# Performance work log

Measured on AMD Instinct MI355X. Metric: run time of the kernel, lower is better.

Reference implementation:

```python
import jax, jax.numpy as jnp
import numpy as np
from jax.scipy.linalg import solve_triangular

X_DIM, N_INEQ, N_EQ = 64, 32, 16
N = X_DIM + N_INEQ      # primal+slack dim = 96
M = N_EQ + N_INEQ       # combined constraint count = 48
GAMMA = 2.0
NUM_STEPS = 10
BOUND = 1000.0          # state_slack_bound
BATCH = 4096


def setup_inputs() -> dict:
    key = jax.random.key(0)
    k1, k2, k3, k4, k5 = jax.random.split(key, 5)
    x = jax.random.normal(k1, (BATCH, N), dtype=jnp.float32)
    parms = jax.random.normal(k2, (BATCH, X_DIM + N_EQ + N_INEQ), dtype=jnp.float32)
    # PSD quadratic objective matrix so Md = gamma/2*I + Hf is PD for Cholesky
    Qh = jax.random.normal(k3, (X_DIM, X_DIM), dtype=jnp.float32) * 0.1
    Q = Qh @ Qh.T + jnp.eye(X_DIM, dtype=jnp.float32)
    A = jax.random.normal(k4, (N_EQ, X_DIM), dtype=jnp.float32) * 0.1
    G = jax.random.normal(k5, (N_INEQ, X_DIM), dtype=jnp.float32) * 0.1
    return {"x": x, "parms": parms, "Q": Q, "A": A, "G": G}


def _prox_g1(xs, parms, Q, A, G):
    # prox of g1(x,s) = f(x) + i_{F(x,s)=0} via 2nd-order obj / 1st-order constraint approx
    def f_single(z, p):
        xv = z[:X_DIM]
        return 0.5 * xv @ Q @ xv + p[:X_DIM] @ xv

    def F_single(z, p):
        xv, s = z[:X_DIM], z[X_DIM:]
        return jnp.concatenate([A @ xv - p[X_DIM:X_DIM + N_EQ],
                                G @ xv + s - p[X_DIM + N_EQ:]])

    # torch version computes JF/QR under no_grad -> stop_gradient here
    JFx = jax.lax.stop_gradient(jax.vmap(jax.jacrev(F_single, argnums=0))(xs, parms))  # [B,M,N]
    Qc, Rc = jnp.linalg.qr(jnp.swapaxes(JFx, 1, 2), mode='complete')  # Qc [B,N,N], Rc [B,N,M]
    Rr = Rc[:, :M, :]       # [B,M,M]
    Qr = Qc[:, :, :M]       # range space  [B,N,M]
    Qn = Qc[:, :, M:]       # null space   [B,N,N-M]

    Hf = jax.vmap(jax.hessian(f_single, argnums=0))(xs, parms)  # [B,N,N]
    Md = (GAMMA / 2) * jnp.eye(N, dtype=xs.dtype) + Hf          # metric defaults to identity
    QTMdQ = jnp.einsum('bni,bnm,bmj->bij', Qn, Md, Qn)          # [B,N-M,N-M]
    Lcho = jnp.linalg.cholesky(QTMdQ)

    Fx = jax.vmap(F_single)(xs, parms)                 # [B,M]
    b = -Fx[..., None] + JFx @ xs[..., None]           # [B,M,1]
    zeta_r = solve_triangular(jnp.swapaxes(Rr, 1, 2), b, lower=True)
    zeta = Qr @ zeta_r                                 # particular solution [B,N,1]

    fg = jax.vmap(jax.grad(f_single, argnums=0))(xs, parms)[..., None]
    zq = Md @ (xs[..., None] - zeta) - (GAMMA / 2) * fg
    zq = jnp.swapaxes(Qn, 1, 2) @ zq
    zq = solve_triangular(Lcho, zq, lower=True)
    zq = solve_triangular(jnp.swapaxes(Lcho, 1, 2), zq, lower=False)
    zq = Qn @ zq
    return (zq + zeta)[..., 0]


def _prox_g2(v):
    # box projection: x in [-BOUND, BOUND], slacks in [0, BOUND]
    l = jnp.concatenate([-BOUND * jnp.ones(X_DIM, dtype=v.dtype),
                         jnp.zeros(N_INEQ, dtype=v.dtype)])
    u = BOUND * jnp.ones(N, dtype=v.dtype)
    return l + jax.nn.relu(u - l - jax.nn.relu(u - v))


def reference(x, parms, Q, A, G):
    y = x
    for _ in range(NUM_STEPS):  # Douglas-Rachford fixed-point iteration
        y = _prox_g1(x, parms, Q, A, G)
        z = _prox_g2(2.0 * y - x)
        x = x + z - y
    return y[:, :X_DIM]  # primal solution estimate
```

## Files before the change

### kernel.cpp

```cpp
#include <hip/hip_runtime.h>


typedef __attribute__((ext_vector_type(8))) short short8v;
typedef __attribute__((ext_vector_type(4))) short short4v;
typedef __attribute__((ext_vector_type(4))) float float4v;

#define MFMA_BF16 __builtin_amdgcn_mfma_f32_16x16x32_bf16

__device__ __forceinline__ void ld4(const float* p, float* d) {
  float4 v = *(const float4*)p;
  d[0] = v.x; d[1] = v.y; d[2] = v.z; d[3] = v.w;
}
__device__ __forceinline__ void st4(float* p, const float* s) {
  *(float4*)p = make_float4(s[0], s[1], s[2], s[3]);
}
__device__ __forceinline__ float fastrcp(float x) {
  float r = __builtin_amdgcn_rcpf(x);
  return r * (2.0f - x * r);
}
__device__ __forceinline__ void mm4(float W[4][4], const float A[4][4], const float B[4][4]) {
  #pragma unroll
  for (int r = 0; r < 4; ++r)
    #pragma unroll
    for (int q = 0; q < 4; ++q) {
      float s = A[r][0]*B[0][q];
      #pragma unroll
      for (int k = 1; k < 4; ++k) s += A[r][k]*B[k][q];
      W[r][q] = s;
    }
}
__device__ __forceinline__ void inv4(float D[4][4]) {
  #pragma unroll
  for (int p = 0; p < 4; ++p) {
    float pi = fastrcp(D[p][p]);
    D[p][p] = pi;
    #pragma unroll
    for (int q = 0; q < 4; ++q) if (q != p) D[p][q] *= pi;
    #pragma unroll
    for (int i = 0; i < 4; ++i) if (i != p) {
      float f = D[i][p];
      #pragma unroll
      for (int q = 0; q < 4; ++q) if (q != p) D[i][q] -= f * D[p][q];
      D[i][p] = -f * pi;
    }
  }
}
__device__ __forceinline__ unsigned short bf16h_rne(float v) {
  unsigned u = __float_as_uint(v);
  unsigned r = u + 0x7FFFu + ((u >> 16) & 1u);
  return (unsigned short)(r >> 16);
}
__device__ __forceinline__ float bf16_back(unsigned short h) {
  return __uint_as_float(((unsigned)h) << 16);
}
__device__ __forceinline__ void split8(const float v[8], short8v &hi, short8v &lo) {
  #pragma unroll
  for (int j = 0; j < 8; ++j) {
    unsigned short h = bf16h_rne(v[j]);
    hi[j] = (short)h;
    lo[j] = (short)bf16h_rne(v[j] - bf16_back(h));
  }
}

__device__ __forceinline__ void gj_step64(const float* __restrict__ src,
                                          float* __restrict__ dst,
                                          int b, int ig, int jg) {
  float D[4][4], C[4][4], R[4][4], T4[4][4], W[4][4];
  #pragma unroll
  for (int r = 0; r < 4; ++r) {
    ld4(&src[(4*b + r)*68 + 4*b],  D[r]);
    ld4(&src[(4*ig + r)*68 + 4*b], C[r]);
    ld4(&src[(4*b + r)*68 + 4*jg], R[r]);
    ld4(&src[(4*ig + r)*68 + 4*jg], T4[r]);
  }
  inv4(D);
  if (ig == b) {
    if (jg == b) {
      #pragma unroll
      for (int r = 0; r < 4; ++r)
        #pragma unroll
        for (int q = 0; q < 4; ++q) W[r][q] = D[r][q];
    } else {
      mm4(W, D, R);
    }
  } else {
    float E[4][4];
    mm4(E, C, D);
    if (jg == b) {
      #pragma unroll
      for (int r = 0; r < 4; ++r)
        #pragma unroll
        for (int q = 0; q < 4; ++q) W[r][q] = -E[r][q];
    } else {
      #pragma unroll
      for (int r = 0; r < 4; ++r)
        #pragma unroll
        for (int q = 0; q < 4; ++q) {
          float s = T4[r][q];
          #pragma unroll
          for (int k = 0; k < 4; ++k) s -= E[r][k] * R[k][q];
          W[r][q] = s;
        }
    }
  }
  #pragma unroll
  for (int r = 0; r < 4; ++r) st4(&dst[(4*ig + r)*68 + 4*jg], W[r]);
  __syncthreads();
}

__device__ __forceinline__ void gj_step48(const float* __restrict__ src,
                                          float* __restrict__ dst,
                                          int b, int tid) {
  const bool act = tid < 144;
  const int ig = tid / 12, jg = tid - (tid / 12) * 12;
  float D[4][4], C[4][4], R[4][4], T4[4][4], W[4][4];
  if (act) {
    #pragma unroll
    for (int r = 0; r < 4; ++r) {
      ld4(&src[(4*b + r)*52 + 4*b],  D[r]);
      ld4(&src[(4*ig + r)*52 + 4*b], C[r]);
      ld4(&src[(4*b + r)*52 + 4*jg], R[r]);
      ld4(&src[(4*ig + r)*52 + 4*jg], T4[r]);
    }
    inv4(D);
    if (ig == b) {
      if (jg == b) {
        #pragma unroll
        for (int r = 0; r < 4; ++r)
          #pragma unroll
          for (int q = 0; q < 4; ++q) W[r][q] = D[r][q];
      } else {
        mm4(W, D, R);
      }
    } else {
      float E[4][4];
      mm4(E, C, D);
      if (jg == b) {
        #pragma unroll
        for (int r = 0; r < 4; ++r)
          #pragma unroll
          for (int q = 0; q < 4; ++q) W[r][q] = -E[r][q];
      } else {
        #pragma unroll
        for (int r = 0; r < 4; ++r)
          #pragma unroll
          for (int q = 0; q < 4; ++q) {
            float s = T4[r][q];
            #pragma unroll
            for (int k = 0; k < 4; ++k) s -= E[r][k] * R[k][q];
            W[r][q] = s;
          }
      }
    }
    #pragma unroll
    for (int r = 0; r < 4; ++r) st4(&dst[(4*ig + r)*52 + 4*jg], W[r]);
  }
  __syncthreads();
}

__global__ __launch_bounds__(256, 1) void prep1_kernel(
    const float* __restrict__ Qg, const float* __restrict__ Ag,
    const float* __restrict__ Gg,
    float* __restrict__ Sg, float* __restrict__ Tg, float* __restrict__ Kig)
{
  __shared__ float sMa[64*68];
  __shared__ float sMb[64*68];
  __shared__ float sK [48*52];
  __shared__ float sJx[48*68];

#define SM_(i,j) sMa[(i)*68+(j)]
#define TT_(i,j) sMb[(i)*48+(j)]
#define SK_(i,j) sK[(i)*52+(j)]
#define JX_(a,k) sJx[(a)*68+(k)]

  const int tid = threadIdx.x;
  const int ig = tid >> 4, jg = tid & 15;

  {
    const float4* A4 = (const float4*)Ag;
    const float4* G4 = (const float4*)Gg;
    {
      int a = tid >> 4, kc = tid & 15;
      float v[4]; ld4((const float*)&A4[tid], v);
      st4(&JX_(a, kc*4), v);
    }
    for (int t = tid; t < 512; t += 256) {
      int a = t >> 4, kc = t & 15;
      float v[4]; ld4((const float*)&G4[t], v);
      st4(&JX_(16 + a, kc*4), v);
    }
    const float4* Q4 = (const float4*)Qg;
    for (int t = tid; t < 1024; t += 256) {
      int i = t >> 4, kc = t & 15;
      float v[4]; ld4((const float*)&Q4[t], v);
      st4(&SM_(i, kc*4), v);
    }
  }
  __syncthreads();
  if (tid < 64) SM_(tid, tid) += 1.0f;
  __syncthreads();

  #pragma unroll 1
  for (int p = 0; p < 8; ++p) {
    gj_step64(sMa, sMb, 2*p,     ig, jg);
    gj_step64(sMb, sMa, 2*p + 1, ig, jg);
  }

  {
    const int i0 = 4*ig, j0 = 3*jg;
    float acc[4][3] = {};
    #pragma unroll 4
    for (int kq = 0; kq < 16; ++kq) {
      float sv[4][4], jv[3][4];
      ld4(&SM_(i0+0, kq*4), sv[0]); ld4(&SM_(i0+1, kq*4), sv[1]);
      ld4(&SM_(i0+2, kq*4), sv[2]); ld4(&SM_(i0+3, kq*4), sv[3]);
      ld4(&JX_(j0+0, kq*4), jv[0]); ld4(&JX_(j0+1, kq*4), jv[1]);
      ld4(&JX_(j0+2, kq*4), jv[2]);
      #pragma unroll
      for (int r = 0; r < 4; ++r)
        #pragma unroll
        for (int c = 0; c < 3; ++c)
          #pragma unroll
          for (int s = 0; s < 4; ++s)
            acc[r][c] += sv[r][s] * jv[c][s];
    }
    __syncthreads();
    #pragma unroll
    for (int r = 0; r < 4; ++r)
      #pragma unroll
      for (int c = 0; c < 3; ++c)
        TT_(i0+r, j0+c) = acc[r][c];
  }
  __syncthreads();

  if (tid < 192) {
    int ag = tid / 12, bg = tid - ag*12;
    int a0 = ag*3, b0 = bg*4;
    float acc[3][4] = {};
    #pragma unroll 4
    for (int k = 0; k < 64; ++k) {
      float4 tb = *(const float4*)&TT_(k,b0);
      #pragma unroll
      for (int r = 0; r < 3; ++r) {
        float jv = JX_(a0 + r, k);
        acc[r][0] += jv*tb.x; acc[r][1] += jv*tb.y;
        acc[r][2] += jv*tb.z; acc[r][3] += jv*tb.w;
      }
    }
    #pragma unroll
    for (int r = 0; r < 3; ++r)
      #pragma unroll
      for (int q = 0; q < 4; ++q) {
        int a = a0 + r, b = b0 + q;
        SK_(a,b) = acc[r][q] + ((a == b && a >= 16) ? 1.0f : 0.0f);
      }
  }
  __syncthreads();

  {
    float* KP = sJx;
    #pragma unroll 1
    for (int p = 0; p < 6; ++p) {
      gj_step48(sK, KP, 2*p,     tid);
      gj_step48(KP, sK, 2*p + 1, tid);
    }
  }

  #pragma unroll 1
  for (int t = tid; t < 1024; t += 256) {
    int i = t >> 4, q = t & 15;
    float v[4]; ld4(&SM_(i, q*4), v); st4(&Sg[i*64 + q*4], v);
  }
  #pragma unroll 1
  for (int t = tid; t < 768; t += 256) {
    int i = t / 12, q = t - 12*(t/12);
    float v[4]; ld4(&TT_(i, q*4), v); st4(&Tg[i*48 + q*4], v);
  }
  #pragma unroll 1
  for (int t = tid; t < 576; t += 256) {
    int k = t / 12, q = t - 12*(t/12);
    float v[4]; ld4(&SK_(k, q*4), v); st4(&Kig[k*48 + q*4], v);
  }
#undef SM_
#undef TT_
#undef SK_
#undef JX_
}

__global__ __launch_bounds__(256, 1) void prep2_kernel(
    const float* __restrict__ Sg, const float* __restrict__ Tg,
    const float* __restrict__ Kig,
    float* __restrict__ Pg, float* __restrict__ Bg)
{
  __shared__ float sT [64*48];
  __shared__ float sKi[48*48];
  __shared__ float sR2[48*96];
  __shared__ float sS [24*64];

  const int tid = threadIdx.x;
  const int b   = blockIdx.x;
  const int r0b = 24 * b;

  #pragma unroll 1
  for (int t = tid; t < 768; t += 256) {
    float v[4]; ld4(&Tg[t*4], v); st4(&sT[t*4], v);
  }
  #pragma unroll 1
  for (int t = tid; t < 576; t += 256) {
    float v[4]; ld4(&Kig[t*4], v); st4(&sKi[t*4], v);
  }
  #pragma unroll 1
  for (int t = tid; t < 384; t += 256) {
    int ri = t >> 4, q = t & 15;
    if (r0b + ri < 64) {
      float v[4]; ld4(&Sg[(r0b + ri)*64 + q*4], v); st4(&sS[ri*64 + q*4], v);
    }
  }
  __syncthreads();

  #pragma unroll 1
  for (int t = tid; t < 48*64; t += 256) {
    int k = t >> 6, c = t & 63;
    float acc = 0.0f;
    #pragma unroll 4
    for (int m = 0; m < 48; m += 4) {
      float kv[4], tv[4];
      ld4(&sKi[k*48 + m], kv); ld4(&sT[c*48 + m], tv);
      acc += kv[0]*tv[0] + kv[1]*tv[1] + kv[2]*tv[2] + kv[3]*tv[3];
    }
    sR2[k*96 + c] = acc;
  }
  #pragma unroll 1
  for (int t = tid; t < 48*32; t += 256) {
    int k = t >> 5, j = t & 31;
    sR2[k*96 + 64 + j] = sKi[k*48 + 16 + j];
  }
  __syncthreads();

  #pragma unroll 1
  for (int t = tid; t < 24*48; t += 256) {
    int c = r0b + t / 48, k = t - 48*(t/48);
    Bg[c*112 + 64 + k] = sR2[k*96 + c];
  }

  #pragma unroll 1
  for (int task = tid; task < 576; task += 256) {
    int ri = task / 24, jq = task - 24*(task/24);
    int i = r0b + ri, j0 = jq*4;
    if (i < 64) {
      float acc[4];
      #pragma unroll
      for (int q = 0; q < 4; ++q)
        acc[q] = (j0 < 64) ? sS[ri*64 + j0 + q] : 0.0f;
      #pragma unroll 4
      for (int m = 0; m < 48; m += 4) {
        float tv[4], rv[4][4];
        ld4(&sT[i*48 + m], tv);
        ld4(&sR2[(m+0)*96 + j0], rv[0]);
        ld4(&sR2[(m+1)*96 + j0], rv[1]);
        ld4(&sR2[(m+2)*96 + j0], rv[2]);
        ld4(&sR2[(m+3)*96 + j0], rv[3]);
        #pragma unroll
        for (int q = 0; q < 4; ++q)
          #pragma unroll
          for (int s = 0; s < 4; ++s)
            acc[q] -= tv[s] * rv[s][q];
      }
      #pragma unroll
      for (int q = 0; q < 4; ++q) {
        int j = j0 + q;
        Pg[i*96 + j] = acc[q];
        if (j < 64) Bg[i*112 + j] = -acc[q];
      }
    } else {
      int a = i - 64;
      #pragma unroll
      for (int q = 0; q < 4; ++q) {
        int j = j0 + q;
        float v = (i == j ? 1.0f : 0.0f) - sR2[(16 + a)*96 + j];
        Pg[i*96 + j] = v;
        if (j < 64) Bg[i*112 + j] = -v;
      }
    }
  }
}

#define EB 16

__global__ __launch_bounds__(384, 1) void iter_kernel(
    const float* __restrict__ xg, const float* __restrict__ pg,
    const float* __restrict__ Pg, const float* __restrict__ Bg,
    float* __restrict__ outg)
{
  __shared__ short sXh[2][EB*104], sXl[2][EB*104];

  const int tid   = threadIdx.x;
  const int gbase = blockIdx.x * EB;
  const int w     = tid >> 6;
  const int lane  = tid & 63;
  const int e     = lane & 15;
  const int g     = lane >> 4;
  const int row0  = 16 * w;
  const int rbase = row0 + 4*g;

  short8v pfh[3], pfl[3];
  #pragma unroll
  for (int kc = 0; kc < 3; ++kc) {
    float v[8];
    const float* src = Pg + (row0 + e)*96 + 32*kc + 8*g;
    ld4(src, v); ld4(src + 4, v + 4);
    split8(v, pfh[kc], pfl[kc]);
  }

  float xo[4];
  ld4(xg + (size_t)(gbase + e)*96 + rbase, xo);
  {
    short4v hv, lv;
    #pragma unroll
    for (int r = 0; r < 4; ++r) {
      unsigned short h = bf16h_rne(xo[r]);
      hv[r] = (short)h;
      lv[r] = (short)bf16h_rne(xo[r] - bf16_back(h));
    }
    *(short4v*)&sXh[0][e*104 + rbase] = hv;
    *(short4v*)&sXl[0][e*104 + rbase] = lv;
  }

  float4v cfrag = {0.f, 0.f, 0.f, 0.f};
  #pragma unroll
  for (int kc = 0; kc < 4; ++kc) {
    const int kbase = 32*kc + 8*g;
    float v[8];
    short8v ah, al, bh, bl;
    if (kbase < 112) {
      const float* src = Bg + (row0 + e)*112 + kbase;
      ld4(src, v); ld4(src + 4, v + 4);
    } else {
      #pragma unroll
      for (int j = 0; j < 8; ++j) v[j] = 0.f;
    }
    split8(v, ah, al);
    if (kbase < 112) {
      const float* src = pg + (size_t)(gbase + e)*112 + kbase;
      ld4(src, v); ld4(src + 4, v + 4);
    } else {
      #pragma unroll
      for (int j = 0; j < 8; ++j) v[j] = 0.f;
    }
    split8(v, bh, bl);
    cfrag = MFMA_BF16(ah, bh, cfrag, 0, 0, 0);
    cfrag = MFMA_BF16(ah, bl, cfrag, 0, 0, 0);
    cfrag = MFMA_BF16(al, bh, cfrag, 0, 0, 0);
  }

  __syncthreads();

  const float lob = (row0 < 64) ? -1000.f : 0.f;
  int cur = 0;

  #pragma unroll 1
  for (int it = 0; it < 10; ++it) {
    const short* xhp = &sXh[cur][0];
    const short* xlp = &sXl[cur][0];
    float4v accs0 = cfrag;
    float4v accs1 = {0.f, 0.f, 0.f, 0.f};
    float4v accs2 = {0.f, 0.f, 0.f, 0.f};
    {
      int off = e*104 + 8*g;
      short8v xh0 = *(const short8v*)&xhp[off];
      short8v xl0 = *(const short8v*)&xlp[off];
      short8v xh1 = *(const short8v*)&xhp[off + 32];
      short8v xl1 = *(const short8v*)&xlp[off + 32];
      short8v xh2 = *(const short8v*)&xhp[off + 64];
      short8v xl2 = *(const short8v*)&xlp[off + 64];
      accs0 = MFMA_BF16(pfh[0], xh0, accs0, 0, 0, 0);
      accs1 = MFMA_BF16(pfh[1], xh1, accs1, 0, 0, 0);
      accs2 = MFMA_BF16(pfh[2], xh2, accs2, 0, 0, 0);
      accs0 = MFMA_BF16(pfh[0], xl0, accs0, 0, 0, 0);
      accs1 = MFMA_BF16(pfh[1], xl1, accs1, 0, 0, 0);
      accs2 = MFMA_BF16(pfh[2], xl2, accs2, 0, 0, 0);
      accs0 = MFMA_BF16(pfl[0], xh0, accs0, 0, 0, 0);
      accs1 = MFMA_BF16(pfl[1], xh1, accs1, 0, 0, 0);
      accs2 = MFMA_BF16(pfl[2], xh2, accs2, 0, 0, 0);
    }
    float4v acc = accs0 + accs1 + accs2;

    if (it < 9) {
      short4v hv, lv;
      #pragma unroll
      for (int r = 0; r < 4; ++r) {
        float y = acc[r];
        float z = fminf(fmaxf(2.f*y - xo[r], lob), 1000.f);
        float xn = xo[r] + z - y;
        xo[r] = xn;
        unsigned short h = bf16h_rne(xn);
        hv[r] = (short)h;
        lv[r] = (short)bf16h_rne(xn - bf16_back(h));
      }
      *(short4v*)&sXh[cur ^ 1][e*104 + rbase] = hv;
      *(short4v*)&sXl[cur ^ 1][e*104 + rbase] = lv;
      __syncthreads();
      cur ^= 1;
    } else {
      if (row0 < 64) {
        *(float4*)&outg[(gbase + e)*64 + rbase] =
            make_float4(acc[0], acc[1], acc[2], acc[3]);
      }
    }
  }
}

extern "C" void kernel_launch(void* const* d_in, const int* in_sizes, int n_in,
                              void* d_out, int out_size, void* d_ws, size_t ws_size,
                              hipStream_t stream) {
  const float* x     = (const float*)d_in[0];
  const float* parms = (const float*)d_in[1];
  const float* Qg    = (const float*)d_in[2];
  const float* Ag    = (const float*)d_in[3];
  const float* Gg    = (const float*)d_in[4];
  float* out = (float*)d_out;

  float* ws  = (float*)d_ws;
  float* Pg  = ws;
  float* Bg  = ws + 9216;
  float* Sg  = ws + 19968;
  float* Tg  = ws + 24064;
  float* Kig = ws + 27136;

  prep1_kernel<<<1, 256, 0, stream>>>(Qg, Ag, Gg, Sg, Tg, Kig);
  prep2_kernel<<<4, 256, 0, stream>>>(Sg, Tg, Kig, Pg, Bg);
  iter_kernel<<<4096 / EB, 384, 0, stream>>>(x, parms, Pg, Bg, out);
}
```

Measured before the change: 54.41 us.

## Halve batch elements per block in iter kernel and keep GJ tiles in registers

The iteration kernel now handles 8 batch elements per block instead of 16, doubling the block count so more CUs are busy. The 16-wide MFMA tiles stay, with the upper 8 columns zero-padded, and occupancy is hinted at 3 blocks per CU. This wastes half of the MFMA work per block and repeats the per-block preload of the P and B matrices. Separately, the Gauss-Jordan steps in the prep kernel keep each thread's own 4x4 tile in registers across steps rather than reloading it from shared memory.

```diff
diff --git a/kernel.cpp b/kernel.cpp
--- a/kernel.cpp
+++ b/kernel.cpp
@@ -62,16 +62,16 @@
   }
 }
 
-__device__ __forceinline__ void gj_step64(const float* __restrict__ src,
-                                          float* __restrict__ dst,
-                                          int b, int ig, int jg) {
-  float D[4][4], C[4][4], R[4][4], T4[4][4], W[4][4];
+__device__ __forceinline__ void gj_step64r(const float* __restrict__ src,
+                                           float* __restrict__ dst,
+                                           int b, int ig, int jg,
+                                           float T4[4][4]) {
+  float D[4][4], C[4][4], R[4][4];
   #pragma unroll
   for (int r = 0; r < 4; ++r) {
-    ld4(&src[(4*b + r)*68 + 4*b],  D[r]);
-    ld4(&src[(4*ig + r)*68 + 4*b], C[r]);
-    ld4(&src[(4*b + r)*68 + 4*jg], R[r]);
-    ld4(&src[(4*ig + r)*68 + 4*jg], T4[r]);
+    ld4(&src[(4*b + r)*68 + 4*b],   D[r]);
+    ld4(&src[(4*ig + r)*68 + 4*b],  C[r]);
+    ld4(&src[(4*b + r)*68 + 4*jg],  R[r]);
   }
   inv4(D);
   if (ig == b) {
@@ -79,9 +79,9 @@
       #pragma unroll
       for (int r = 0; r < 4; ++r)
         #pragma unroll
-        for (int q = 0; q < 4; ++q) W[r][q] = D[r][q];
-    } else {
-      mm4(W, D, R);
+        for (int q = 0; q < 4; ++q) T4[r][q] = D[r][q];
+    } else {
+      mm4(T4, D, R);
     }
   } else {
     float E[4][4];
@@ -90,7 +90,7 @@
       #pragma unroll
       for (int r = 0; r < 4; ++r)
         #pragma unroll
-        for (int q = 0; q < 4; ++q) W[r][q] = -E[r][q];
+        for (int q = 0; q < 4; ++q) T4[r][q] = -E[r][q];
     } else {
       #pragma unroll
       for (int r = 0; r < 4; ++r)
@@ -99,28 +99,26 @@
           float s = T4[r][q];
           #pragma unroll
           for (int k = 0; k < 4; ++k) s -= E[r][k] * R[k][q];
-          W[r][q] = s;
+          T4[r][q] = s;
         }
     }
   }
   #pragma unroll
-  for (int r = 0; r < 4; ++r) st4(&dst[(4*ig + r)*68 + 4*jg], W[r]);
-  __syncthreads();
-}
-
-__device__ __forceinline__ void gj_step48(const float* __restrict__ src,
-                                          float* __restrict__ dst,
-                                          int b, int tid) {
-  const bool act = tid < 144;
-  const int ig = tid / 12, jg = tid - (tid / 12) * 12;
-  float D[4][4], C[4][4], R[4][4], T4[4][4], W[4][4];
+  for (int r = 0; r < 4; ++r) st4(&dst[(4*ig + r)*68 + 4*jg], T4[r]);
+  __syncthreads();
+}
+
+__device__ __forceinline__ void gj_step48r(const float* __restrict__ src,
+                                           float* __restrict__ dst,
+                                           int b, int ig, int jg, bool act,
+                                           float T4[4][4]) {
   if (act) {
+    float D[4][4], C[4][4], R[4][4];
     #pragma unroll
     for (int r = 0; r < 4; ++r) {
-      ld4(&src[(4*b + r)*52 + 4*b],  D[r]);
-      ld4(&src[(4*ig + r)*52 + 4*b], C[r]);
-      ld4(&src[(4*b + r)*52 + 4*jg], R[r]);
-      ld4(&src[(4*ig + r)*52 + 4*jg], T4[r]);
+      ld4(&src[(4*b + r)*52 + 4*b],   D[r]);
+      ld4(&src[(4*ig + r)*52 + 4*b],  C[r]);
+      ld4(&src[(4*b + r)*52 + 4*jg],  R[r]);
     }
     inv4(D);
     if (ig == b) {
@@ -128,9 +126,9 @@
         #pragma unroll
         for (int r = 0; r < 4; ++r)
           #pragma unroll
-          for (int q = 0; q < 4; ++q) W[r][q] = D[r][q];
+          for (int q = 0; q < 4; ++q) T4[r][q] = D[r][q];
       } else {
-        mm4(W, D, R);
+        mm4(T4, D, R);
       }
     } else {
       float E[4][4];
@@ -139,7 +137,7 @@
         #pragma unroll
         for (int r = 0; r < 4; ++r)
           #pragma unroll
-          for (int q = 0; q < 4; ++q) W[r][q] = -E[r][q];
+          for (int q = 0; q < 4; ++q) T4[r][q] = -E[r][q];
       } else {
         #pragma unroll
         for (int r = 0; r < 4; ++r)
@@ -148,12 +146,12 @@
             float s = T4[r][q];
             #pragma unroll
             for (int k = 0; k < 4; ++k) s -= E[r][k] * R[k][q];
-            W[r][q] = s;
+            T4[r][q] = s;
           }
       }
     }
     #pragma unroll
-    for (int r = 0; r < 4; ++r) st4(&dst[(4*ig + r)*52 + 4*jg], W[r]);
+    for (int r = 0; r < 4; ++r) st4(&dst[(4*ig + r)*52 + 4*jg], T4[r]);
   }
   __syncthreads();
 }
@@ -200,10 +198,15 @@
   if (tid < 64) SM_(tid, tid) += 1.0f;
   __syncthreads();
 
-  #pragma unroll 1
-  for (int p = 0; p < 8; ++p) {
-    gj_step64(sMa, sMb, 2*p,     ig, jg);
-    gj_step64(sMb, sMa, 2*p + 1, ig, jg);
+  {
+    float T64[4][4];
+    #pragma unroll
+    for (int r = 0; r < 4; ++r) ld4(&SM_(4*ig + r, 4*jg), T64[r]);
+    #pragma unroll 1
+    for (int p = 0; p < 8; ++p) {
+      gj_step64r(sMa, sMb, 2*p,     ig, jg, T64);
+      gj_step64r(sMb, sMa, 2*p + 1, ig, jg, T64);
+    }
   }
 
   {
@@ -259,10 +262,17 @@
 
   {
     float* KP = sJx;
+    const bool act = tid < 144;
+    const int ig48 = tid / 12, jg48 = tid - (tid / 12) * 12;
+    float T48[4][4];
+    if (act) {
+      #pragma unroll
+      for (int r = 0; r < 4; ++r) ld4(&SK_(4*ig48 + r, 4*jg48), T48[r]);
+    }
     #pragma unroll 1
     for (int p = 0; p < 6; ++p) {
-      gj_step48(sK, KP, 2*p,     tid);
-      gj_step48(KP, sK, 2*p + 1, tid);
+      gj_step48r(sK, KP, 2*p,     ig48, jg48, act, T48);
+      gj_step48r(KP, sK, 2*p + 1, ig48, jg48, act, T48);
     }
   }
 
@@ -385,14 +395,14 @@
   }
 }
 
-#define EB 16
-
-__global__ __launch_bounds__(384, 1) void iter_kernel(
+#define EB 8
+
+__global__ __launch_bounds__(384, 3) void iter_kernel(
     const float* __restrict__ xg, const float* __restrict__ pg,
     const float* __restrict__ Pg, const float* __restrict__ Bg,
     float* __restrict__ outg)
 {
-  __shared__ short sXh[2][EB*104], sXl[2][EB*104];
+  __shared__ short sXh[2][16*104], sXl[2][16*104];
 
   const int tid   = threadIdx.x;
   const int gbase = blockIdx.x * EB;
@@ -403,6 +413,12 @@
   const int row0  = 16 * w;
   const int rbase = row0 + 4*g;
 
+  for (int t = tid; t < 8*104; t += 384) {
+    int e2 = 8 + t / 104, k = t - 104 * (t / 104);
+    sXh[0][e2*104 + k] = 0; sXl[0][e2*104 + k] = 0;
+    sXh[1][e2*104 + k] = 0; sXl[1][e2*104 + k] = 0;
+  }
+
   short8v pfh[3], pfl[3];
   #pragma unroll
   for (int kc = 0; kc < 3; ++kc) {
@@ -412,9 +428,9 @@
     split8(v, pfh[kc], pfl[kc]);
   }
 
-  float xo[4];
-  ld4(xg + (size_t)(gbase + e)*96 + rbase, xo);
-  {
+  float xo[4] = {0.f, 0.f, 0.f, 0.f};
+  if (e < 8) {
+    ld4(xg + (size_t)(gbase + e)*96 + rbase, xo);
     short4v hv, lv;
     #pragma unroll
     for (int r = 0; r < 4; ++r) {
@@ -440,7 +456,7 @@
       for (int j = 0; j < 8; ++j) v[j] = 0.f;
     }
     split8(v, ah, al);
-    if (kbase < 112) {
+    if (kbase < 112 && e < 8) {
       const float* src = pg + (size_t)(gbase + e)*112 + kbase;
       ld4(src, v); ld4(src + 4, v + 4);
     } else {
@@ -486,23 +502,25 @@
     float4v acc = accs0 + accs1 + accs2;
 
     if (it < 9) {
-      short4v hv, lv;
-      #pragma unroll
-      for (int r = 0; r < 4; ++r) {
-        float y = acc[r];
-        float z = fminf(fmaxf(2.f*y - xo[r], lob), 1000.f);
-        float xn = xo[r] + z - y;
-        xo[r] = xn;
-        unsigned short h = bf16h_rne(xn);
-        hv[r] = (short)h;
-        lv[r] = (short)bf16h_rne(xn - bf16_back(h));
-      }
-      *(short4v*)&sXh[cur ^ 1][e*104 + rbase] = hv;
-      *(short4v*)&sXl[cur ^ 1][e*104 + rbase] = lv;
+      if (e < 8) {
+        short4v hv, lv;
+        #pragma unroll
+        for (int r = 0; r < 4; ++r) {
+          float y = acc[r];
+          float z = fminf(fmaxf(2.f*y - xo[r], lob), 1000.f);
+          float xn = xo[r] + z - y;
+          xo[r] = xn;
+          unsigned short h = bf16h_rne(xn);
+          hv[r] = (short)h;
+          lv[r] = (short)bf16h_rne(xn - bf16_back(h));
+        }
+        *(short4v*)&sXh[cur ^ 1][e*104 + rbase] = hv;
+        *(short4v*)&sXl[cur ^ 1][e*104 + rbase] = lv;
+      }
       __syncthreads();
       cur ^= 1;
     } else {
-      if (row0 < 64) {
+      if (row0 < 64 && e < 8) {
         *(float4*)&outg[(gbase + e)*64 + rbase] =
             make_float4(acc[0], acc[1], acc[2], acc[3]);
       }
```

Result: slower. 66.52 us (+22.3%).

## Replace Gauss-Jordan inverse of Q+I with parallel Chebyshev iteration on MFMA

Applied to the files above, without the earlier changes.

The single-block 64x64 Gauss-Jordan inversion of Q+I and the subsequent S·Jx^T product are replaced by a 14-block kernel. Each block runs a fixed 20-step Chebyshev iteration using split-bf16 MFMA matvecs, solving for 8 columns of either the inverse or of (Q+I)^-1 Jx^T. Eigenvalue bounds come from Gershgorin row sums. The K-inverse Gauss-Jordan moves into a separate single-block kernel. This spreads the serial preprocessing across many CUs but adds a kernel launch. Accuracy depends on the fixed iteration count converging for the given spectrum.

```diff
diff --git a/kernel.cpp b/kernel.cpp
--- a/kernel.cpp
+++ b/kernel.cpp
@@ -62,50 +62,130 @@
   }
 }
 
-__device__ __forceinline__ void gj_step64(const float* __restrict__ src,
-                                          float* __restrict__ dst,
-                                          int b, int ig, int jg) {
-  float D[4][4], C[4][4], R[4][4], T4[4][4], W[4][4];
+#define CHEB_ITERS 20
+
+__global__ __launch_bounds__(256, 1) void prepA_kernel(
+    const float* __restrict__ Qg, const float* __restrict__ Ag,
+    const float* __restrict__ Gg,
+    float* __restrict__ Sg, float* __restrict__ Tg)
+{
+  __shared__ short sDh[2][16*104], sDl[2][16*104];
+  __shared__ float sRed[68];
+
+  const int tid  = threadIdx.x;
+  const int w    = tid >> 6, lane = tid & 63;
+  const int e    = lane & 15, g = lane >> 4;
+  const int row0 = 16*w, rbase = row0 + 4*g;
+  const int colg = 8*(int)blockIdx.x + e;
+
+  if (tid < 64) {
+    float s = 1.0f;
+    #pragma unroll 4
+    for (int kq = 0; kq < 16; ++kq) {
+      float v[4]; ld4(&Qg[tid*64 + kq*4], v);
+      s += fabsf(v[0]) + fabsf(v[1]) + fabsf(v[2]) + fabsf(v[3]);
+    }
+    sRed[tid] = s;
+  }
+  __syncthreads();
+  if (tid == 0) {
+    float b = sRed[0];
+    #pragma unroll 4
+    for (int k = 1; k < 64; ++k) b = fmaxf(b, sRed[k]);
+    sRed[64] = b;
+  }
+
+  short8v mah[2], mal[2];
+  #pragma unroll
+  for (int ks = 0; ks < 2; ++ks) {
+    const int kb = 32*ks + 8*g;
+    float v[8];
+    ld4(&Qg[(row0+e)*64 + kb], v);
+    ld4(&Qg[(row0+e)*64 + kb + 4], v + 4);
+    #pragma unroll
+    for (int j = 0; j < 8; ++j)
+      if (row0 + e == kb + j) v[j] += 1.0f;
+    split8(v, mah[ks], mal[ks]);
+  }
+
+  __syncthreads();
+  const float B     = sRed[64];
+  const float theta = 0.5f*(B + 1.0f);
+  const float delta = 0.5f*(B - 1.0f);
+  const float sigma = theta / delta;
+  float rho = delta / theta;
+
+  float xv[4] = {0.f,0.f,0.f,0.f}, rv[4], dv[4];
   #pragma unroll
   for (int r = 0; r < 4; ++r) {
-    ld4(&src[(4*b + r)*68 + 4*b],  D[r]);
-    ld4(&src[(4*ig + r)*68 + 4*b], C[r]);
-    ld4(&src[(4*b + r)*68 + 4*jg], R[r]);
-    ld4(&src[(4*ig + r)*68 + 4*jg], T4[r]);
-  }
-  inv4(D);
-  if (ig == b) {
-    if (jg == b) {
-      #pragma unroll
-      for (int r = 0; r < 4; ++r)
-        #pragma unroll
-        for (int q = 0; q < 4; ++q) W[r][q] = D[r][q];
+    float bb = 0.f;
+    if (e < 8) {
+      if (colg < 64) {
+        bb = (rbase + r == colg) ? 1.0f : 0.0f;
+      } else {
+        int jr = colg - 64;
+        bb = (jr < 16) ? Ag[jr*64 + rbase + r] : Gg[(jr-16)*64 + rbase + r];
+      }
+    }
+    rv[r] = bb;
+    dv[r] = bb / theta;
+  }
+  {
+    short4v hv, lv;
+    #pragma unroll
+    for (int r = 0; r < 4; ++r) {
+      unsigned short h = bf16h_rne(dv[r]);
+      hv[r] = (short)h;
+      lv[r] = (short)bf16h_rne(dv[r] - bf16_back(h));
+    }
+    *(short4v*)&sDh[0][e*104 + rbase] = hv;
+    *(short4v*)&sDl[0][e*104 + rbase] = lv;
+  }
+  __syncthreads();
+
+  int cur = 0;
+  #pragma unroll 1
+  for (int it = 0; it < CHEB_ITERS; ++it) {
+    float4v acc = {0.f,0.f,0.f,0.f};
+    const short* dh = &sDh[cur][0];
+    const short* dl = &sDl[cur][0];
+    #pragma unroll
+    for (int ks = 0; ks < 2; ++ks) {
+      int off = e*104 + 32*ks + 8*g;
+      short8v bh = *(const short8v*)&dh[off];
+      short8v bl = *(const short8v*)&dl[off];
+      acc = MFMA_BF16(mah[ks], bh, acc, 0, 0, 0);
+      acc = MFMA_BF16(mah[ks], bl, acc, 0, 0, 0);
+      acc = MFMA_BF16(mal[ks], bh, acc, 0, 0, 0);
+    }
+    float rhon = 1.0f / (2.0f*sigma - rho);
+    float ca = rhon * rho, cb = 2.0f*rhon/delta;
+    short4v hv, lv;
+    #pragma unroll
+    for (int r = 0; r < 4; ++r) {
+      xv[r] += dv[r];
+      rv[r] -= acc[r];
+      dv[r] = ca*dv[r] + cb*rv[r];
+      unsigned short h = bf16h_rne(dv[r]);
+      hv[r] = (short)h;
+      lv[r] = (short)bf16h_rne(dv[r] - bf16_back(h));
+    }
+    rho = rhon;
+    *(short4v*)&sDh[cur^1][e*104 + rbase] = hv;
+    *(short4v*)&sDl[cur^1][e*104 + rbase] = lv;
+    __syncthreads();
+    cur ^= 1;
+  }
+
+  if (e < 8) {
+    if (colg < 64) {
+      *(float4*)&Sg[colg*64 + rbase] = make_float4(xv[0], xv[1], xv[2], xv[3]);
     } else {
-      mm4(W, D, R);
-    }
-  } else {
-    float E[4][4];
-    mm4(E, C, D);
-    if (jg == b) {
-      #pragma unroll
-      for (int r = 0; r < 4; ++r)
-        #pragma unroll
-        for (int q = 0; q < 4; ++q) W[r][q] = -E[r][q];
-    } else {
-      #pragma unroll
-      for (int r = 0; r < 4; ++r)
-        #pragma unroll
-        for (int q = 0; q < 4; ++q) {
-          float s = T4[r][q];
-          #pragma unroll
-          for (int k = 0; k < 4; ++k) s -= E[r][k] * R[k][q];
-          W[r][q] = s;
-        }
-    }
-  }
-  #pragma unroll
-  for (int r = 0; r < 4; ++r) st4(&dst[(4*ig + r)*68 + 4*jg], W[r]);
-  __syncthreads();
+      int j = colg - 64;
+      #pragma unroll
+      for (int r = 0; r < 4; ++r) Tg[(rbase + r)*48 + j] = xv[r];
+    }
+  }
 }
 
 __device__ __forceinline__ void gj_step48(const float* __restrict__ src,
@@ -158,23 +238,19 @@
   __syncthreads();
 }
 
-__global__ __launch_bounds__(256, 1) void prep1_kernel(
-    const float* __restrict__ Qg, const float* __restrict__ Ag,
-    const float* __restrict__ Gg,
-    float* __restrict__ Sg, float* __restrict__ Tg, float* __restrict__ Kig)
+__global__ __launch_bounds__(256, 1) void prepB_kernel(
+    const float* __restrict__ Ag, const float* __restrict__ Gg,
+    const float* __restrict__ Tg, float* __restrict__ Kig)
 {
-  __shared__ float sMa[64*68];
-  __shared__ float sMb[64*68];
+  __shared__ float sT [64*48];
   __shared__ float sK [48*52];
   __shared__ float sJx[48*68];
 
-#define SM_(i,j) sMa[(i)*68+(j)]
-#define TT_(i,j) sMb[(i)*48+(j)]
+#define TT_(i,j) sT[(i)*48+(j)]
 #define SK_(i,j) sK[(i)*52+(j)]
 #define JX_(a,k) sJx[(a)*68+(k)]
 
   const int tid = threadIdx.x;
-  const int ig = tid >> 4, jg = tid & 15;
 
   {
     const float4* A4 = (const float4*)Ag;
@@ -189,47 +265,9 @@
       float v[4]; ld4((const float*)&G4[t], v);
       st4(&JX_(16 + a, kc*4), v);
     }
-    const float4* Q4 = (const float4*)Qg;
-    for (int t = tid; t < 1024; t += 256) {
-      int i = t >> 4, kc = t & 15;
-      float v[4]; ld4((const float*)&Q4[t], v);
-      st4(&SM_(i, kc*4), v);
-    }
-  }
-  __syncthreads();
-  if (tid < 64) SM_(tid, tid) += 1.0f;
-  __syncthreads();
-
-  #pragma unroll 1
-  for (int p = 0; p < 8; ++p) {
-    gj_step64(sMa, sMb, 2*p,     ig, jg);
-    gj_step64(sMb, sMa, 2*p + 1, ig, jg);
-  }
-
-  {
-    const int i0 = 4*ig, j0 = 3*jg;
-    float acc[4][3] = {};
-    #pragma unroll 4
-    for (int kq = 0; kq < 16; ++kq) {
-      float sv[4][4], jv[3][4];
-      ld4(&SM_(i0+0, kq*4), sv[0]); ld4(&SM_(i0+1, kq*4), sv[1]);
-      ld4(&SM_(i0+2, kq*4), sv[2]); ld4(&SM_(i0+3, kq*4), sv[3]);
-      ld4(&JX_(j0+0, kq*4), jv[0]); ld4(&JX_(j0+1, kq*4), jv[1]);
-      ld4(&JX_(j0+2, kq*4), jv[2]);
-      #pragma unroll
-      for (int r = 0; r < 4; ++r)
-        #pragma unroll
-        for (int c = 0; c < 3; ++c)
-          #pragma unroll
-          for (int s = 0; s < 4; ++s)
-            acc[r][c] += sv[r][s] * jv[c][s];
-    }
-    __syncthreads();
-    #pragma unroll
-    for (int r = 0; r < 4; ++r)
-      #pragma unroll
-      for (int c = 0; c < 3; ++c)
-        TT_(i0+r, j0+c) = acc[r][c];
+    for (int t = tid; t < 768; t += 256) {
+      float v[4]; ld4(&Tg[t*4], v); st4(&sT[t*4], v);
+    }
   }
   __syncthreads();
 
@@ -267,21 +305,10 @@
   }
 
   #pragma unroll 1
-  for (int t = tid; t < 1024; t += 256) {
-    int i = t >> 4, q = t & 15;
-    float v[4]; ld4(&SM_(i, q*4), v); st4(&Sg[i*64 + q*4], v);
-  }
-  #pragma unroll 1
-  for (int t = tid; t < 768; t += 256) {
-    int i = t / 12, q = t - 12*(t/12);
-    float v[4]; ld4(&TT_(i, q*4), v); st4(&Tg[i*48 + q*4], v);
-  }
-  #pragma unroll 1
   for (int t = tid; t < 576; t += 256) {
     int k = t / 12, q = t - 12*(t/12);
     float v[4]; ld4(&SK_(k, q*4), v); st4(&Kig[k*48 + q*4], v);
   }
-#undef SM_
 #undef TT_
 #undef SK_
 #undef JX_
@@ -527,7 +554,8 @@
   float* Tg  = ws + 24064;
   float* Kig = ws + 27136;
 
-  prep1_kernel<<<1, 256, 0, stream>>>(Qg, Ag, Gg, Sg, Tg, Kig);
+  prepA_kernel<<<14, 256, 0, stream>>>(Qg, Ag, Gg, Sg, Tg);
+  prepB_kernel<<<1, 256, 0, stream>>>(Ag, Gg, Tg, Kig);
   prep2_kernel<<<4, 256, 0, stream>>>(Sg, Tg, Kig, Pg, Bg);
   iter_kernel<<<4096 / EB, 384, 0, stream>>>(x, parms, Pg, Bg, out);
 }
```

New measurement: 52.57 us. -3.4%, faster.
